# Performance work log

Measured on AMD Instinct MI355X. Metric: run time of the kernel, lower is better.

The kernel has to match this reference:

```python
import jax, jax.numpy as jnp
import numpy as np

B, N, A, O, D, Q, H = 64, 4, 1024, 128, 256, 256, 128
NEG_INF = -1e30


def setup_inputs() -> dict:
    key = jax.random.key(0)
    ks = jax.random.split(key, 8)
    q = jax.random.normal(ks[0], (B, N, 1, Q), dtype=jnp.float32)
    att1 = jax.random.uniform(ks[1], (B, N, A, O), dtype=jnp.float32)
    obj_reps = jax.random.normal(ks[2], (B, O, D), dtype=jnp.float32)
    tags_attention = jax.random.randint(ks[3], (B, N, A), 0, 2, dtype=jnp.int32)
    W1 = jax.random.normal(ks[4], (D + Q, H), dtype=jnp.float32) / np.sqrt(D + Q)
    b1 = jnp.zeros((H,), dtype=jnp.float32)
    W2 = jax.random.normal(ks[5], (H, 1), dtype=jnp.float32) / np.sqrt(H)
    b2 = jnp.zeros((1,), dtype=jnp.float32)
    return {"q": q, "att1": att1, "obj_reps": obj_reps,
            "tags_attention": tags_attention,
            "W1": W1, "b1": b1, "W2": W2, "b2": b2, "t": 1}


def reference(q, att1, obj_reps, tags_attention, W1, b1, W2, b2, t):
    # v: [B,N,A,D] = att1 [B,N,A,O] @ obj_reps [B,O,D]
    v = jnp.einsum('bnao,bod->bnad', att1, obj_reps)
    # q broadcast over token dim A, concat -> [B,N,A,D+Q]
    q_proj = jnp.broadcast_to(q, v.shape[:3] + (q.shape[-1],))
    vq = jnp.concatenate([v, q_proj], axis=-1)
    # FCNet: Linear + ReLU (dropout is identity at inference)
    joint_repr = jax.nn.relu(vq @ W1 + b1)          # [B,N,A,H]
    logits = (joint_repr @ W2 + b2)[..., 0]          # [B,N,A]
    # temperature-scaled masked softmax over tokens
    masked = jnp.where(tags_attention > 0, logits / t, NEG_INF)
    att2 = jax.nn.softmax(masked, axis=-1)           # [B,N,A]
    # attention_last: [B,N,O] = att2 [B,N,1,A] @ att1 [B,N,A,O]
    return jnp.einsum('bna,bnao->bno', att2, att1)
```

## Files before the change

### kernel.cpp

```cpp
#include <hip/hip_runtime.h>
#include <math.h>

#define Bc 64
#define Nc 4
#define Ac 1024
#define Oc 128
#define Dc 256
#define Qc 256
#define Hc 128
#define BN (Bc*Nc)

using f4     = __attribute__((ext_vector_type(4))) float;
using f32x4  = __attribute__((ext_vector_type(4))) float;
using short8 = __attribute__((ext_vector_type(8))) short;
using us4    = __attribute__((ext_vector_type(4))) unsigned short;

__device__ inline float decode_t(const void* p) {
    int i = *(const int*)p;
    if (i >= 1 && i <= 1000000) return (float)i;
    return __int_as_float(i);
}

__device__ inline unsigned short bf16_rne(float x) {
    unsigned u = __builtin_bit_cast(unsigned, x);
    u += 0x7FFFu + ((u >> 16) & 1u);
    return (unsigned short)(u >> 16);
}

__device__ inline void split_bf16(float x, unsigned short& hi, unsigned short& lo) {
    unsigned u = __builtin_bit_cast(unsigned, x);
    hi = (unsigned short)(u >> 16);
    float hif = __builtin_bit_cast(float, u & 0xFFFF0000u);
    float lof = x - hif;
    lo = (unsigned short)(__builtin_bit_cast(unsigned, lof) >> 16);
}

__global__ __launch_bounds__(256) void prep_M_kernel(
    const float* __restrict__ obj, const float* __restrict__ W1,
    unsigned short* __restrict__ Mt_hi, unsigned short* __restrict__ Mt_lo)
{
    __shared__ float w_s[32][36];
    __shared__ float obj_sT[32][68];

    const int t  = threadIdx.x;
    const int tx = t & 15;
    const int ty = t >> 4;
    const int h0 = blockIdx.x * 32;
    const int o0 = blockIdx.y * 64;
    const int b  = blockIdx.z;
    const int r8 = t >> 3, c8 = t & 7;

    const float* objb = obj + ((size_t)b * Oc + o0) * Dc;

    float acc[2][4];
    #pragma unroll
    for (int i = 0; i < 2; i++)
        #pragma unroll
        for (int j = 0; j < 4; j++) acc[i][j] = 0.f;

    f4 wv  = *(const f4*)(W1 + (size_t)r8 * Hc + h0 + c8 * 4);
    f4 ov0 = *(const f4*)(objb + (size_t)r8 * Dc + c8 * 4);
    f4 ov1 = *(const f4*)(objb + (size_t)(r8 + 32) * Dc + c8 * 4);

    for (int ko = 0; ko < 8; ++ko) {
        *(f4*)&w_s[r8][c8 * 4] = wv;
        obj_sT[c8 * 4 + 0][r8] = ov0[0];
        obj_sT[c8 * 4 + 1][r8] = ov0[1];
        obj_sT[c8 * 4 + 2][r8] = ov0[2];
        obj_sT[c8 * 4 + 3][r8] = ov0[3];
        obj_sT[c8 * 4 + 0][r8 + 32] = ov1[0];
        obj_sT[c8 * 4 + 1][r8 + 32] = ov1[1];
        obj_sT[c8 * 4 + 2][r8 + 32] = ov1[2];
        obj_sT[c8 * 4 + 3][r8 + 32] = ov1[3];
        __syncthreads();
        if (ko < 7) {
            wv  = *(const f4*)(W1 + (size_t)((ko + 1) * 32 + r8) * Hc + h0 + c8 * 4);
            ov0 = *(const f4*)(objb + (size_t)r8 * Dc + (ko + 1) * 32 + c8 * 4);
            ov1 = *(const f4*)(objb + (size_t)(r8 + 32) * Dc + (ko + 1) * 32 + c8 * 4);
        }
        #pragma unroll 4
        for (int k = 0; k < 32; k++) {
            float a0 = w_s[k][ty * 2];
            float a1 = w_s[k][ty * 2 + 1];
            f4 bv = *(const f4*)&obj_sT[k][tx * 4];
            #pragma unroll
            for (int j = 0; j < 4; j++) {
                acc[0][j] += a0 * bv[j];
                acc[1][j] += a1 * bv[j];
            }
        }
        __syncthreads();
    }

    #pragma unroll
    for (int i = 0; i < 2; i++) {
        us4 hi, lo;
        #pragma unroll
        for (int j = 0; j < 4; j++) {
            unsigned short h16, l16;
            split_bf16(acc[i][j], h16, l16);
            hi[j] = h16; lo[j] = l16;
        }
        size_t ofs = ((size_t)b * Hc + h0 + ty * 2 + i) * Oc + o0 + tx * 4;
        *(us4*)(Mt_hi + ofs) = hi;
        *(us4*)(Mt_lo + ofs) = lo;
    }
}

__global__ __launch_bounds__(512) void prep_qb_kernel(
    const float* __restrict__ q, const float* __restrict__ W1,
    const float* __restrict__ b1, float* __restrict__ qb)
{
    __shared__ float qs[256];
    __shared__ float red[4][128];
    const int t = threadIdx.x;
    const int bn = blockIdx.x;

    if (t < 256) qs[t] = q[bn * Qc + t];
    __syncthreads();

    const int h = t & 127, kq = t >> 7;
    float acc = 0.f;
    const float* w = W1 + (size_t)(Dc + kq * 64) * Hc + h;
    #pragma unroll 8
    for (int d = 0; d < 64; ++d)
        acc += qs[kq * 64 + d] * w[(size_t)d * Hc];
    red[kq][h] = acc;
    __syncthreads();

    if (t < 128)
        qb[bn * Hc + t] = b1[t] + red[0][t] + red[1][t] + red[2][t] + red[3][t];
}

__global__ __launch_bounds__(1024, 4) void main_kernel(
    const float* __restrict__ att1, const int* __restrict__ tags,
    const unsigned short* __restrict__ Mt_hi, const unsigned short* __restrict__ Mt_lo,
    const float* __restrict__ qb, const float* __restrict__ W2,
    const float* __restrict__ b2, const void* __restrict__ tptr,
    float* __restrict__ out)
{
    __shared__ unsigned short A_s[2][128][136];
    __shared__ float part2[128][9];
    __shared__ float part3[8][132];
    __shared__ float e_s[128];
    __shared__ float qb_s[128], w2_s[128];
    __shared__ float zfin[2];

    const int t    = threadIdx.x;
    const int wave = t >> 6;
    const int lane = t & 63;
    const int l15  = lane & 15;
    const int quad = lane >> 4;
    const int bn = blockIdx.x;
    const int b  = bn >> 2;
    const int rowg = (wave >> 3) * 64;
    const int hw   = (wave & 7) * 16;

    const float* att_bn = att1 + (size_t)bn * Ac * Oc;

    f4 sv[4];
    #pragma unroll
    for (int s = 0; s < 4; s++) {
        int idx = t + 1024 * s;
        sv[s] = *(const f4*)(att_bn + (size_t)idx * 4);
    }

    const size_t brow = ((size_t)b * Hc + hw + l15) * Oc;
    short8 Bh[4], Bl[4];
    #pragma unroll
    for (int ks = 0; ks < 4; ks++) {
        const int ko = ks * 32 + quad * 8;
        Bh[ks] = *(const short8*)(Mt_hi + brow + ko);
        Bl[ks] = *(const short8*)(Mt_lo + brow + ko);
    }

    if (t < 128) { qb_s[t] = qb[bn * Hc + t]; w2_s[t] = W2[t]; }
    int tg_cur = (t < 128) ? tags[(size_t)bn * Ac + t] : 0;
    const float b2v  = b2[0];
    const float tval = decode_t(tptr);

    float z_reg = 0.f, out_reg = 0.f;

    for (int tile = 0; tile < 8; ++tile) {
        const int buf = tile & 1;
        const float* tile_ptr = att_bn + (size_t)tile * 128 * Oc;

        #pragma unroll
        for (int s = 0; s < 4; s++) {
            int idx = t + 1024 * s;
            int r = idx >> 5, c4 = idx & 31;
            us4 h4;
            #pragma unroll
            for (int j = 0; j < 4; j++) h4[j] = bf16_rne(sv[s][j]);
            *(us4*)&A_s[buf][r][c4 * 4] = h4;
        }
        __syncthreads();

        int tg_next = 0;
        if (tile < 7) {
            const float* np = att_bn + (size_t)(tile + 1) * 128 * Oc;
            #pragma unroll
            for (int s = 0; s < 4; s++) {
                int idx = t + 1024 * s;
                sv[s] = *(const f4*)(np + (size_t)idx * 4);
            }
            if (t < 128) tg_next = tags[(size_t)bn * Ac + (tile + 1) * 128 + t];
        }

        f32x4 acc[4];
        #pragma unroll
        for (int i = 0; i < 4; i++) acc[i] = (f32x4)(0.f);
        #pragma unroll
        for (int ks = 0; ks < 4; ks++) {
            const int ko = ks * 32 + quad * 8;
            #pragma unroll
            for (int i = 0; i < 4; i++) {
                short8 ah = *(const short8*)&A_s[buf][rowg + i * 16 + l15][ko];
                acc[i] = __builtin_amdgcn_mfma_f32_16x16x32_bf16(ah, Bh[ks], acc[i], 0, 0, 0);
                acc[i] = __builtin_amdgcn_mfma_f32_16x16x32_bf16(ah, Bl[ks], acc[i], 0, 0, 0);
            }
        }

        {
            const float qbv = qb_s[hw + l15], w2v = w2_s[hw + l15];
            float p[4][4];
            #pragma unroll
            for (int i = 0; i < 4; i++)
                #pragma unroll
                for (int r = 0; r < 4; r++) {
                    float v = acc[i][r] + qbv;
                    v = v > 0.f ? v : 0.f;
                    p[i][r] = v * w2v;
                }
            #pragma unroll
            for (int m = 1; m <= 8; m <<= 1)
                #pragma unroll
                for (int i = 0; i < 4; i++)
                    #pragma unroll
                    for (int r = 0; r < 4; r++)
                        p[i][r] += __shfl_xor(p[i][r], m);
            if (l15 == 0) {
                #pragma unroll
                for (int i = 0; i < 4; i++)
                    #pragma unroll
                    for (int r = 0; r < 4; r++)
                        part2[rowg + i * 16 + quad * 4 + r][wave & 7] = p[i][r];
            }
        }
        __syncthreads();

        if (t < 128) {
            float sum = b2v;
            #pragma unroll
            for (int x = 0; x < 8; x++) sum += part2[t][x];
            float logit = sum / tval;
            float e = (tg_cur > 0) ? __expf(logit) : 0.f;
            e_s[t] = e;
            z_reg += e;
        }
        __syncthreads();

        {
            const int o  = t & 127;
            const int g  = t >> 7;
            const float* ab = tile_ptr + (size_t)(g * 16) * Oc + o;
            float accum = 0.f;
            #pragma unroll
            for (int a = 0; a < 16; a++)
                accum += e_s[g * 16 + a] * ab[(size_t)a * Oc];
            part3[g][o] = accum;
        }
        __syncthreads();

        if (t < 128) {
            float s = 0.f;
            #pragma unroll
            for (int g = 0; g < 8; g++) s += part3[g][t];
            out_reg += s;
        }
        tg_cur = tg_next;
    }

    __syncthreads();
    if (t < 128) {
        float z = z_reg;
        #pragma unroll
        for (int off = 32; off > 0; off >>= 1) z += __shfl_down(z, off);
        if (lane == 0) zfin[wave] = z;
    }
    __syncthreads();
    if (t < 128) {
        float Z = zfin[0] + zfin[1];
        out[(size_t)bn * Oc + t] = out_reg / Z;
    }
}

extern "C" void kernel_launch(void* const* d_in, const int* in_sizes, int n_in,
                              void* d_out, int out_size, void* d_ws, size_t ws_size,
                              hipStream_t stream)
{
    (void)in_sizes; (void)n_in; (void)out_size; (void)ws_size;

    const float* q    = (const float*)d_in[0];
    const float* att1 = (const float*)d_in[1];
    const float* obj  = (const float*)d_in[2];
    const int*   tags = (const int*)d_in[3];
    const float* W1   = (const float*)d_in[4];
    const float* b1   = (const float*)d_in[5];
    const float* W2   = (const float*)d_in[6];
    const float* b2   = (const float*)d_in[7];
    const void*  tptr = d_in[8];
    float* out = (float*)d_out;

    char* wsb = (char*)d_ws;
    unsigned short* Mt_hi = (unsigned short*)wsb;
    unsigned short* Mt_lo = (unsigned short*)(wsb + (size_t)2*1024*1024);
    float* qbuf = (float*)(wsb + (size_t)4*1024*1024);

    prep_M_kernel<<<dim3(4, 2, Bc), 256, 0, stream>>>(obj, W1, Mt_hi, Mt_lo);
    prep_qb_kernel<<<dim3(BN), 512, 0, stream>>>(q, W1, b1, qbuf);
    main_kernel<<<dim3(BN), 1024, 0, stream>>>(att1, tags, Mt_hi, Mt_lo,
                                               qbuf, W2, b2, tptr, out);
}
```

Measured before the change: 246.9 us.

## Split each (b,n) row across two blocks and add a finalize reduction kernel

The main kernel now launches two 512-thread blocks per (b,n), each handling half of the 1024 tokens in 64-row tiles with a single LDS buffer. Each block writes a partial output vector and a partial softmax normalizer, and a new finalize kernel combines the two halves and divides. The goal is more blocks (512 instead of 256) to fill the 256 CUs and smaller blocks for better occupancy. The cost is an extra kernel launch, a round-trip of partial results through global memory, and dropping the A-tile double buffer. The softmax has no max subtraction, so adding the two halves stays consistent.

```diff
diff --git a/kernel.cpp b/kernel.cpp
--- a/kernel.cpp
+++ b/kernel.cpp
@@ -132,37 +132,37 @@
         qb[bn * Hc + t] = b1[t] + red[0][t] + red[1][t] + red[2][t] + red[3][t];
 }
 
-__global__ __launch_bounds__(1024, 4) void main_kernel(
+__global__ __launch_bounds__(512, 4) void main_half_kernel(
     const float* __restrict__ att1, const int* __restrict__ tags,
     const unsigned short* __restrict__ Mt_hi, const unsigned short* __restrict__ Mt_lo,
     const float* __restrict__ qb, const float* __restrict__ W2,
     const float* __restrict__ b2, const void* __restrict__ tptr,
-    float* __restrict__ out)
-{
-    __shared__ unsigned short A_s[2][128][136];
-    __shared__ float part2[128][9];
-    __shared__ float part3[8][132];
-    __shared__ float e_s[128];
+    float* __restrict__ out_part, float* __restrict__ z_part)
+{
+    __shared__ unsigned short A_s[64][136];
+    __shared__ float part2[64][9];
+    __shared__ float part3[4][132];
+    __shared__ float e_s[64];
     __shared__ float qb_s[128], w2_s[128];
-    __shared__ float zfin[2];
 
     const int t    = threadIdx.x;
+    const int lane = t & 63;
     const int wave = t >> 6;
-    const int lane = t & 63;
     const int l15  = lane & 15;
     const int quad = lane >> 4;
-    const int bn = blockIdx.x;
-    const int b  = bn >> 2;
-    const int rowg = (wave >> 3) * 64;
-    const int hw   = (wave & 7) * 16;
-
-    const float* att_bn = att1 + (size_t)bn * Ac * Oc;
+    const int blk  = blockIdx.x;
+    const int bn   = blk >> 1;
+    const int half = blk & 1;
+    const int b    = bn >> 2;
+    const int hw   = wave * 16;
+
+    const float* att_half = att1 + ((size_t)bn * Ac + half * 512) * Oc;
 
     f4 sv[4];
     #pragma unroll
     for (int s = 0; s < 4; s++) {
-        int idx = t + 1024 * s;
-        sv[s] = *(const f4*)(att_bn + (size_t)idx * 4);
+        int idx = t + 512 * s;
+        sv[s] = *(const f4*)(att_half + (size_t)idx * 4);
     }
 
     const size_t brow = ((size_t)b * Hc + hw + l15) * Oc;
@@ -175,36 +175,41 @@
     }
 
     if (t < 128) { qb_s[t] = qb[bn * Hc + t]; w2_s[t] = W2[t]; }
-    int tg_cur = (t < 128) ? tags[(size_t)bn * Ac + t] : 0;
+    int tg_cur = (t < 64) ? tags[(size_t)bn * Ac + half * 512 + t] : 0;
     const float b2v  = b2[0];
     const float tval = decode_t(tptr);
 
     float z_reg = 0.f, out_reg = 0.f;
 
     for (int tile = 0; tile < 8; ++tile) {
-        const int buf = tile & 1;
-        const float* tile_ptr = att_bn + (size_t)tile * 128 * Oc;
-
+        const float* tile_ptr = att_half + (size_t)tile * 64 * Oc;
+
+        if (tile > 0 && t < 128) {
+            float s = 0.f;
+            #pragma unroll
+            for (int g = 0; g < 4; g++) s += part3[g][t];
+            out_reg += s;
+        }
         #pragma unroll
         for (int s = 0; s < 4; s++) {
-            int idx = t + 1024 * s;
+            int idx = t + 512 * s;
             int r = idx >> 5, c4 = idx & 31;
             us4 h4;
             #pragma unroll
             for (int j = 0; j < 4; j++) h4[j] = bf16_rne(sv[s][j]);
-            *(us4*)&A_s[buf][r][c4 * 4] = h4;
+            *(us4*)&A_s[r][c4 * 4] = h4;
         }
         __syncthreads();
 
         int tg_next = 0;
         if (tile < 7) {
-            const float* np = att_bn + (size_t)(tile + 1) * 128 * Oc;
+            const float* np = tile_ptr + 64 * Oc;
             #pragma unroll
             for (int s = 0; s < 4; s++) {
-                int idx = t + 1024 * s;
+                int idx = t + 512 * s;
                 sv[s] = *(const f4*)(np + (size_t)idx * 4);
             }
-            if (t < 128) tg_next = tags[(size_t)bn * Ac + (tile + 1) * 128 + t];
+            if (t < 64) tg_next = tags[(size_t)bn * Ac + half * 512 + (tile + 1) * 64 + t];
         }
 
         f32x4 acc[4];
@@ -215,7 +220,7 @@
             const int ko = ks * 32 + quad * 8;
             #pragma unroll
             for (int i = 0; i < 4; i++) {
-                short8 ah = *(const short8*)&A_s[buf][rowg + i * 16 + l15][ko];
+                short8 ah = *(const short8*)&A_s[i * 16 + l15][ko];
                 acc[i] = __builtin_amdgcn_mfma_f32_16x16x32_bf16(ah, Bh[ks], acc[i], 0, 0, 0);
                 acc[i] = __builtin_amdgcn_mfma_f32_16x16x32_bf16(ah, Bl[ks], acc[i], 0, 0, 0);
             }
@@ -244,12 +249,12 @@
                 for (int i = 0; i < 4; i++)
                     #pragma unroll
                     for (int r = 0; r < 4; r++)
-                        part2[rowg + i * 16 + quad * 4 + r][wave & 7] = p[i][r];
+                        part2[i * 16 + quad * 4 + r][wave] = p[i][r];
             }
         }
         __syncthreads();
 
-        if (t < 128) {
+        if (t < 64) {
             float sum = b2v;
             #pragma unroll
             for (int x = 0; x < 8; x++) sum += part2[t][x];
@@ -261,8 +266,8 @@
         __syncthreads();
 
         {
-            const int o  = t & 127;
-            const int g  = t >> 7;
+            const int o = t & 127;
+            const int g = t >> 7;
             const float* ab = tile_ptr + (size_t)(g * 16) * Oc + o;
             float accum = 0.f;
             #pragma unroll
@@ -271,28 +276,34 @@
             part3[g][o] = accum;
         }
         __syncthreads();
-
-        if (t < 128) {
-            float s = 0.f;
-            #pragma unroll
-            for (int g = 0; g < 8; g++) s += part3[g][t];
-            out_reg += s;
-        }
         tg_cur = tg_next;
     }
 
-    __syncthreads();
     if (t < 128) {
+        float s = 0.f;
+        #pragma unroll
+        for (int g = 0; g < 4; g++) s += part3[g][t];
+        out_reg += s;
+        out_part[(size_t)blk * 128 + t] = out_reg;
+    }
+    if (t < 64) {
         float z = z_reg;
         #pragma unroll
         for (int off = 32; off > 0; off >>= 1) z += __shfl_down(z, off);
-        if (lane == 0) zfin[wave] = z;
-    }
-    __syncthreads();
-    if (t < 128) {
-        float Z = zfin[0] + zfin[1];
-        out[(size_t)bn * Oc + t] = out_reg / Z;
-    }
+        if (t == 0) z_part[blk] = z;
+    }
+}
+
+__global__ __launch_bounds__(128) void finalize_kernel(
+    const float* __restrict__ out_part, const float* __restrict__ z_part,
+    float* __restrict__ out)
+{
+    const int bn = blockIdx.x;
+    const int t  = threadIdx.x;
+    const float Z = z_part[bn * 2] + z_part[bn * 2 + 1];
+    const float v = out_part[(size_t)(bn * 2) * 128 + t]
+                  + out_part[(size_t)(bn * 2 + 1) * 128 + t];
+    out[(size_t)bn * 128 + t] = v / Z;
 }
 
 extern "C" void kernel_launch(void* const* d_in, const int* in_sizes, int n_in,
@@ -309,16 +320,20 @@
     const float* b1   = (const float*)d_in[5];
     const float* W2   = (const float*)d_in[6];
     const float* b2   = (const float*)d_in[7];
-    const void*  tptr = d_in[8];
+    const void*  tptr = (const void*)d_in[8];
     float* out = (float*)d_out;
 
     char* wsb = (char*)d_ws;
     unsigned short* Mt_hi = (unsigned short*)wsb;
     unsigned short* Mt_lo = (unsigned short*)(wsb + (size_t)2*1024*1024);
-    float* qbuf = (float*)(wsb + (size_t)4*1024*1024);
+    float* qbuf     = (float*)(wsb + (size_t)4*1024*1024);
+    float* out_part = (float*)(wsb + (size_t)5*1024*1024);
+    float* z_part   = (float*)(wsb + (size_t)6*1024*1024);
 
     prep_M_kernel<<<dim3(4, 2, Bc), 256, 0, stream>>>(obj, W1, Mt_hi, Mt_lo);
     prep_qb_kernel<<<dim3(BN), 512, 0, stream>>>(q, W1, b1, qbuf);
-    main_kernel<<<dim3(BN), 1024, 0, stream>>>(att1, tags, Mt_hi, Mt_lo,
-                                               qbuf, W2, b2, tptr, out);
-}
+    main_half_kernel<<<dim3(2 * BN), 512, 0, stream>>>(att1, tags, Mt_hi, Mt_lo,
+                                                       qbuf, W2, b2, tptr,
+                                                       out_part, z_part);
+    finalize_kernel<<<dim3(BN), 128, 0, stream>>>(out_part, z_part, out);
+}
```

After: 242.7 us. No clear change (-1.7%).
